# Kernel optimization log

Hardware: AMD Instinct MI355X
Metric: run time of the kernel (lower is better)

## Reference

```python
import jax, jax.numpy as jnp
import numpy as np

SQRT_2 = 1.414213
RT = 1.0  # Disk sets self.rt = 1.0
N_KPTS = 8192
M_KPTS = 8192
F_DIM = 256  # SuperPoint descriptor dim


def setup_inputs() -> dict:
    key = jax.random.key(0)
    k0, k1, k2, k3 = jax.random.split(key, 4)
    d0 = jax.random.normal(k0, (1, F_DIM, N_KPTS), dtype=jnp.float32)
    d1 = jax.random.normal(k1, (1, F_DIM, M_KPTS), dtype=jnp.float32)
    # distance_matrix assumes L2-normalized descriptors (normalize over F axis)
    d0 = d0 / jnp.linalg.norm(d0, axis=1, keepdims=True)
    d1 = d1 / jnp.linalg.norm(d1, axis=1, keepdims=True)
    kpts0 = jax.random.uniform(k2, (1, N_KPTS, 2), dtype=jnp.float32) * 480.0
    kpts1 = jax.random.uniform(k3, (1, M_KPTS, 2), dtype=jnp.float32) * 480.0
    return {"descriptors0": d0, "descriptors1": d1,
            "keypoints0": kpts0, "keypoints1": kpts1}


def _ratio_nn(dist):
    """Per-row nearest neighbor + Lowe ratio test. dist: [A, B].
    Returns (nn_idx [A] int32, pass_mask [A] bool)."""
    neg2, idx2 = jax.lax.top_k(-dist, 2)  # two smallest distances per row
    d1, d2 = -neg2[:, 0], -neg2[:, 1]
    return idx2[:, 0], (d1 / d2) < RT


def reference(descriptors0, descriptors1, keypoints0, keypoints1):
    fs0 = descriptors0[0].T  # [N, F]
    fs1 = descriptors1[0].T  # [M, F]
    # cosine -> L2-on-unit-sphere distance matrix, clamped as in the source
    dist = SQRT_2 * jnp.sqrt(jnp.clip(1.0 - fs0 @ fs1.T, 1e-6, None))  # [N, M]

    fwd_nn, fwd_ok = _ratio_nn(dist)    # [N]
    bck_nn, bck_ok = _ratio_nn(dist.T)  # [M]

    # mutual NN: (i, fwd_nn[i]) is kept iff the backward pass produced the
    # flipped pair (i, fwd_nn[i]) too -> same as counts==2 in the torch merge
    n = fs0.shape[0]
    mutual = fwd_ok & bck_ok[fwd_nn] & (bck_nn[fwd_nn] == jnp.arange(n))

    indices0 = jnp.where(mutual, fwd_nn, -1)[None, :].astype(jnp.int32)  # [1, N]
    mscores0 = jnp.where(indices0 > 0, 1, 0).astype(jnp.int32)           # [1, N]
    matches1 = jnp.full(keypoints1.shape[:-1], -1, dtype=jnp.int32)      # [1, M]
    mscores1 = jnp.zeros(keypoints1.shape[:-1], dtype=keypoints1.dtype)  # [1, M]
    return indices0, matches1, mscores0, mscores1
```

## Files before the change

kernel.cpp:

```cpp
#include <hip/hip_runtime.h>
#include <float.h>

#define NPTS 8192
#define MPTS 8192
#define FDIM 256

#define BM 128
#define BN 128
#define BK 64
#define TCT (MPTS / BN)
#define TRT (NPTS / BM)

typedef unsigned short ushort_t;
typedef unsigned int u32;
typedef __attribute__((ext_vector_type(8))) short short8;
typedef __attribute__((ext_vector_type(4))) float floatx4;

struct T2 { float s1, s2; int i1; };

__device__ __forceinline__ T2 t2_sent() { T2 a; a.s1 = -FLT_MAX; a.s2 = -FLT_MAX; a.i1 = 0; return a; }

__device__ __forceinline__ T2 t2_merge(T2 a, T2 b) {
    T2 r;
    r.s1 = fmaxf(a.s1, b.s1);
    r.i1 = (b.s1 > a.s1) ? b.i1 : a.i1;
    r.s2 = fmaxf(fminf(a.s1, b.s1), fmaxf(a.s2, b.s2));
    return r;
}
__device__ __forceinline__ T2 t2_make4(float v0, float v1, float v2, float v3,
                                       int i0, int i1_, int i2, int i3) {
    float lo01 = fminf(v0, v1), hi01 = fmaxf(v0, v1);
    float lo23 = fminf(v2, v3), hi23 = fmaxf(v2, v3);
    int a01 = (v1 > v0) ? i1_ : i0;
    int a23 = (v3 > v2) ? i3 : i2;
    T2 r;
    r.s1 = fmaxf(hi01, hi23);
    r.i1 = (hi23 > hi01) ? a23 : a01;
    r.s2 = fmaxf(fminf(hi01, hi23), fmaxf(lo01, lo23));
    return r;
}
__device__ __forceinline__ float4 t2_pack(T2 a) {
    return make_float4(a.s1, a.s2, __int_as_float(a.i1), 0.0f);
}
__device__ __forceinline__ T2 t2_unpack(float4 v) {
    T2 a; a.s1 = v.x; a.s2 = v.y; a.i1 = __float_as_int(v.z); return a;
}
__device__ __forceinline__ T2 t2_shfl_xor(T2 a, int m) {
    T2 r; r.s1 = __shfl_xor(a.s1, m); r.s2 = __shfl_xor(a.s2, m); r.i1 = __shfl_xor(a.i1, m);
    return r;
}

__device__ __forceinline__ float bf2f(ushort_t u) {
    union { u32 i; float f; } v; v.i = ((u32)u) << 16; return v.f;
}
__device__ __forceinline__ ushort_t f2bf_rtne(float x) {
    u32 u = __float_as_uint(x);
    u32 r = u + 0x7FFFu + ((u >> 16) & 1u);
    return (ushort_t)(r >> 16);
}

__global__ __launch_bounds__(256) void transpose_split(
    const float* __restrict__ s0, const float* __restrict__ s1,
    ushort_t* __restrict__ hi0, ushort_t* __restrict__ lo0,
    ushort_t* __restrict__ hi1, ushort_t* __restrict__ lo1)
{
    __shared__ ushort_t hiS[64][66];
    __shared__ ushort_t loS[64][66];
    const float* src = blockIdx.z ? s1 : s0;
    ushort_t* hiT = blockIdx.z ? hi1 : hi0;
    ushort_t* loT = blockIdx.z ? lo1 : lo0;
    const int t = threadIdx.x;
    const int n0 = blockIdx.x * 64, f0 = blockIdx.y * 64;

#pragma unroll
    for (int p = 0; p < 4; p++) {
        int fl = (t >> 4) + p * 16;
        int nl = (t & 15) * 4;
        float4 x = *(const float4*)&src[(size_t)(f0 + fl) * NPTS + n0 + nl];
        float xs[4] = {x.x, x.y, x.z, x.w};
#pragma unroll
        for (int e = 0; e < 4; e++) {
            ushort_t hb = f2bf_rtne(xs[e]);
            ushort_t lb = f2bf_rtne(xs[e] - bf2f(hb));
            hiS[nl + e][fl] = hb;
            loS[nl + e][fl] = lb;
        }
    }
    __syncthreads();
#pragma unroll
    for (int p = 0; p < 8; p++) {
        int nl = (t >> 5) + p * 8;
        int fp = (t & 31) * 2;
        u32 hw = (u32)hiS[nl][fp] | ((u32)hiS[nl][fp + 1] << 16);
        u32 lw = (u32)loS[nl][fp] | ((u32)loS[nl][fp + 1] << 16);
        size_t o = (size_t)(n0 + nl) * FDIM + f0 + fp;
        *(u32*)&hiT[o] = hw;
        *(u32*)&loT[o] = lw;
    }
}

#define GLDS(g, l) __builtin_amdgcn_global_load_lds( \
    (const __attribute__((address_space(1))) void*)(g), \
    (__attribute__((address_space(3))) void*)(l), 16, 0, 0)

__global__ __launch_bounds__(256, 2) void gemm_top2(
    const ushort_t* __restrict__ hiA, const ushort_t* __restrict__ loA,
    const ushort_t* __restrict__ hiB, const ushort_t* __restrict__ loB,
    float4* __restrict__ rowPart, float4* __restrict__ colPart)
{
    __shared__ char smem[65536];
    ushort_t* Ah = (ushort_t*)smem;
    ushort_t* Bh = (ushort_t*)(smem + 16384);
    ushort_t* Al = (ushort_t*)(smem + 32768);
    ushort_t* Bl = (ushort_t*)(smem + 49152);
    float* scrS1 = (float*)smem;
    float* scrS2 = (float*)(smem + 8448);
    int*   scrI  = (int*)(smem + 16896);
    float4* redC = (float4*)(smem + 25600);

    const int t = threadIdx.x;
    const int lane = t & 63, lc = lane & 15, q = lane >> 4;
    const int w = t >> 6, wx = w & 1, wy = w >> 1;
    const int ctile = blockIdx.x, rtile = blockIdx.y;
    const int n0 = rtile * BM, m0 = ctile * BN;

    floatx4 acc[4][4];
#pragma unroll
    for (int i = 0; i < 4; i++)
#pragma unroll
        for (int j = 0; j < 4; j++) acc[i][j] = (floatx4)0.0f;

    int srcOff[4];
#pragma unroll
    for (int cc = 0; cc < 4; cc++) {
        int L = cc * 256 + t;
        int row = L >> 3;
        int g = (L & 7) ^ (row & 7);
        srcOff[cc] = row * FDIM + g * 8;
    }
    const ushort_t* bAh = hiA + (size_t)n0 * FDIM;
    const ushort_t* bAl = loA + (size_t)n0 * FDIM;
    const ushort_t* bBh = hiB + (size_t)m0 * FDIM;
    const ushort_t* bBl = loB + (size_t)m0 * FDIM;

    int aoff[4][2], boff[4][2];
#pragma unroll
    for (int i = 0; i < 4; i++) {
        int ra = wy * 64 + i * 16 + lc;
        int rb = wx * 64 + i * 16 + lc;
#pragma unroll
        for (int s = 0; s < 2; s++) {
            aoff[i][s] = ra * BK + (((s * 4 + q) ^ (ra & 7)) * 8);
            boff[i][s] = rb * BK + (((s * 4 + q) ^ (rb & 7)) * 8);
        }
    }

    for (int k0 = 0; k0 < FDIM; k0 += BK) {
        if (k0) __syncthreads();
#pragma unroll
        for (int cc = 0; cc < 4; cc++) {
            int so = srcOff[cc] + k0;
            int ld = (cc * 256 + t) * 8;
            GLDS(bAh + so, Ah + ld);
            GLDS(bBh + so, Bh + ld);
            GLDS(bAl + so, Al + ld);
            GLDS(bBl + so, Bl + ld);
        }
        __syncthreads();

#pragma unroll
        for (int s = 0; s < 2; s++) {
            short8 ah[4], bh[4], al[4], bl[4];
#pragma unroll
            for (int i = 0; i < 4; i++) {
                ah[i] = *(const short8*)&Ah[aoff[i][s]];
                al[i] = *(const short8*)&Al[aoff[i][s]];
            }
#pragma unroll
            for (int j = 0; j < 4; j++) {
                bh[j] = *(const short8*)&Bh[boff[j][s]];
                bl[j] = *(const short8*)&Bl[boff[j][s]];
            }
#pragma unroll
            for (int i = 0; i < 4; i++)
#pragma unroll
                for (int j = 0; j < 4; j++) {
                    acc[i][j] = __builtin_amdgcn_mfma_f32_16x16x32_bf16(ah[i], bh[j], acc[i][j], 0, 0, 0);
                    acc[i][j] = __builtin_amdgcn_mfma_f32_16x16x32_bf16(ah[i], bl[j], acc[i][j], 0, 0, 0);
                    acc[i][j] = __builtin_amdgcn_mfma_f32_16x16x32_bf16(al[i], bh[j], acc[i][j], 0, 0, 0);
                }
        }
    }

    T2 colT[4];
#pragma unroll
    for (int j = 0; j < 4; j++) colT[j] = t2_sent();
    T2 rowT[4][4];

    const int cb = m0 + wx * 64 + lc;
#pragma unroll
    for (int i = 0; i < 4; i++) {
#pragma unroll
        for (int r = 0; r < 4; r++)
            rowT[i][r] = t2_make4(acc[i][0][r], acc[i][1][r], acc[i][2][r], acc[i][3][r],
                                  cb, cb + 16, cb + 32, cb + 48);
        const int rb = n0 + wy * 64 + i * 16 + q * 4;
#pragma unroll
        for (int j = 0; j < 4; j++)
            colT[j] = t2_merge(colT[j],
                t2_make4(acc[i][j][0], acc[i][j][1], acc[i][j][2], acc[i][j][3],
                         rb, rb + 1, rb + 2, rb + 3));
    }

#pragma unroll
    for (int j = 0; j < 4; j++) {
        colT[j] = t2_merge(colT[j], t2_shfl_xor(colT[j], 16));
        colT[j] = t2_merge(colT[j], t2_shfl_xor(colT[j], 32));
        if (q == 0) redC[(wx * 64 + j * 16 + lc) * 2 + wy] = t2_pack(colT[j]);
    }

#pragma unroll
    for (int round = 0; round < 2; round++) {
        __syncthreads();
        if (wy == round) {
#pragma unroll
            for (int i = 0; i < 4; i++)
#pragma unroll
                for (int r = 0; r < 4; r++) {
                    int row = i * 16 + q * 4 + r;
                    int col = (lc << 1) | wx;
                    int slot = row * 33 + ((col + row + 9 * q) & 31);
                    scrS1[slot] = rowT[i][r].s1;
                    scrS2[slot] = rowT[i][r].s2;
                    scrI[slot]  = rowT[i][r].i1;
                }
        }
        __syncthreads();
        {
            int row = t >> 2, chunk = t & 3;
            T2 a = t2_sent();
#pragma unroll
            for (int s = 0; s < 8; s++) {
                int slot = row * 33 + ((chunk << 3) | s);
                T2 b; b.s1 = scrS1[slot]; b.s2 = scrS2[slot]; b.i1 = scrI[slot];
                a = t2_merge(a, b);
            }
            a = t2_merge(a, t2_shfl_xor(a, 1));
            a = t2_merge(a, t2_shfl_xor(a, 2));
            if (chunk == 0)
                rowPart[(size_t)ctile * NPTS + n0 + round * 64 + row] = t2_pack(a);
        }
    }

    __syncthreads();
    if (t < 128) {
        T2 m = t2_unpack(redC[t * 2 + 0]);
        m = t2_merge(m, t2_unpack(redC[t * 2 + 1]));
        colPart[(size_t)rtile * MPTS + m0 + t] = t2_pack(m);
    }
}

__global__ __launch_bounds__(256) void reduce_final(
    const float4* __restrict__ rowPart, const float4* __restrict__ colPart,
    float* __restrict__ out)
{
    __shared__ float4 sh[4][64];
    __shared__ int shFwd[64];
    __shared__ int shOk[64];
    const int t = threadIdx.x, nl = t & 63, sub = t >> 6;
    const int n = blockIdx.x * 64 + nl;

    T2 a = t2_sent();
#pragma unroll
    for (int k = 0; k < 16; k++)
        a = t2_merge(a, t2_unpack(rowPart[(size_t)(sub * 16 + k) * NPTS + n]));
    sh[sub][nl] = t2_pack(a);
    __syncthreads();
    if (t < 64) {
        T2 r = t2_unpack(sh[0][t]);
        r = t2_merge(r, t2_unpack(sh[1][t]));
        r = t2_merge(r, t2_unpack(sh[2][t]));
        r = t2_merge(r, t2_unpack(sh[3][t]));
        float c1 = fmaxf(1.0f - r.s1, 1e-6f), c2 = fmaxf(1.0f - r.s2, 1e-6f);
        float d1 = 1.414213f * sqrtf(c1), d2 = 1.414213f * sqrtf(c2);
        shFwd[t] = r.i1;
        shOk[t]  = ((d1 / d2) < 1.0f) ? 1 : 0;
    }
    __syncthreads();
    const int fw = shFwd[nl];
    T2 c = t2_sent();
#pragma unroll
    for (int k = 0; k < 16; k++)
        c = t2_merge(c, t2_unpack(colPart[(size_t)(sub * 16 + k) * MPTS + fw]));
    sh[sub][nl] = t2_pack(c);
    __syncthreads();
    if (t < 64) {
        T2 r = t2_unpack(sh[0][t]);
        r = t2_merge(r, t2_unpack(sh[1][t]));
        r = t2_merge(r, t2_unpack(sh[2][t]));
        r = t2_merge(r, t2_unpack(sh[3][t]));
        float c1 = fmaxf(1.0f - r.s1, 1e-6f), c2 = fmaxf(1.0f - r.s2, 1e-6f);
        float d1 = 1.414213f * sqrtf(c1), d2 = 1.414213f * sqrtf(c2);
        bool bok = (d1 / d2) < 1.0f;
        int nn = blockIdx.x * 64 + t;
        bool mutual = (shOk[t] != 0) && bok && (r.i1 == nn);
        int idx0 = mutual ? shFwd[t] : -1;
        out[nn]             = (float)idx0;
        out[NPTS + nn]      = -1.0f;
        out[2 * NPTS + nn]  = (idx0 > 0) ? 1.0f : 0.0f;
        out[3 * NPTS + nn]  = 0.0f;
    }
}

extern "C" void kernel_launch(void* const* d_in, const int* in_sizes, int n_in,
                              void* d_out, int out_size, void* d_ws, size_t ws_size,
                              hipStream_t stream)
{
    const float* d0 = (const float*)d_in[0];
    const float* d1 = (const float*)d_in[1];

    char* ws = (char*)d_ws;
    const size_t matB = (size_t)NPTS * FDIM * sizeof(ushort_t);
    ushort_t* hiA = (ushort_t*)(ws);
    ushort_t* loA = (ushort_t*)(ws + matB);
    ushort_t* hiB = (ushort_t*)(ws + 2 * matB);
    ushort_t* loB = (ushort_t*)(ws + 3 * matB);
    char* p = ws + 4 * matB;
    const size_t rowBytes = (size_t)TCT * NPTS * sizeof(float4);
    float4* rowPart = (float4*)p;
    float4* colPart = (float4*)(p + rowBytes);

    dim3 gt(NPTS / 64, FDIM / 64, 2);
    transpose_split<<<gt, 256, 0, stream>>>(d0, d1, hiA, loA, hiB, loB);

    dim3 g1(TCT, TRT);
    gemm_top2<<<g1, 256, 0, stream>>>(hiA, loA, hiB, loB, rowPart, colPart);
    reduce_final<<<NPTS / 64, 256, 0, stream>>>(rowPart, colPart, (float*)d_out);
}
```

Baseline: 179.8 us.

## Use 256x256 tiles with double-buffered LDS pipeline and 8-wave blocks

Enlarges the GEMM tile to 256x256 with 512 threads and BK=32. Global-to-LDS loads for the next K step are double-buffered and issued during MFMA phases, using explicit waitcnt, barriers and priority hints. Larger tiles cut redundant operand reloads and halve the partial top-2 outputs that reduce_final must merge. In exchange, LDS use grows to 128 KB and each thread carries 128 accumulator registers, which limits occupancy.

New measurement: 243.8 us. 35.6% more time.

```diff
diff --git a/kernel.cpp b/kernel.cpp
--- a/kernel.cpp
+++ b/kernel.cpp
@@ -5,9 +5,10 @@
 #define MPTS 8192
 #define FDIM 256
 
-#define BM 128
-#define BN 128
-#define BK 64
+#define BM 256
+#define BN 256
+#define BK 32
+#define KSTEPS (FDIM / BK)
 #define TCT (MPTS / BN)
 #define TRT (NPTS / BM)
 
@@ -103,136 +104,178 @@
     (const __attribute__((address_space(1))) void*)(g), \
     (__attribute__((address_space(3))) void*)(l), 16, 0, 0)
 
-__global__ __launch_bounds__(256, 2) void gemm_top2(
+#define STAGE(k0v, bufp, cc) do { \
+    int _so = srcOff[cc] + (k0v); \
+    char* _lb = (bufp) + ldsOff[cc]; \
+    GLDS(bAh + _so, _lb); \
+    GLDS(bBh + _so, _lb + 16384); \
+    GLDS(bAl + _so, _lb + 32768); \
+    GLDS(bBl + _so, _lb + 49152); \
+} while (0)
+
+#define READ_PH1(Pb) do { \
+    _Pragma("unroll") for (int i = 0; i < 4; i++) { \
+        ah[i] = *(const short8*)((Pb) + aBase + i * 1024); \
+        al[i] = *(const short8*)((Pb) + 32768 + aBase + i * 1024); \
+    } \
+    _Pragma("unroll") for (int j = 0; j < 4; j++) { \
+        bh[j] = *(const short8*)((Pb) + 16384 + bBase + j * 1024); \
+        bl[j] = *(const short8*)((Pb) + 49152 + bBase + j * 1024); \
+    } \
+} while (0)
+
+#define MFMA16(AH, AL, IOFF) do { \
+    _Pragma("unroll") for (int i = 0; i < 4; i++) \
+    _Pragma("unroll") for (int j = 0; j < 4; j++) { \
+        acc[(IOFF) + i][j] = __builtin_amdgcn_mfma_f32_16x16x32_bf16(AH[i], bh[j], acc[(IOFF) + i][j], 0, 0, 0); \
+        acc[(IOFF) + i][j] = __builtin_amdgcn_mfma_f32_16x16x32_bf16(AH[i], bl[j], acc[(IOFF) + i][j], 0, 0, 0); \
+        acc[(IOFF) + i][j] = __builtin_amdgcn_mfma_f32_16x16x32_bf16(AL[i], bh[j], acc[(IOFF) + i][j], 0, 0, 0); \
+    } \
+} while (0)
+
+#define KSTEP(ksv, Pb, Qb) do { \
+    const int kn_ = ((ksv) + 1) * BK; \
+    STAGE(kn_, Qb, 0); \
+    asm volatile("s_waitcnt vmcnt(4)" ::: "memory"); \
+    __builtin_amdgcn_s_barrier(); \
+    READ_PH1(Pb); \
+    asm volatile("s_waitcnt lgkmcnt(0)" ::: "memory"); \
+    __builtin_amdgcn_sched_barrier(0); \
+    __builtin_amdgcn_s_setprio(1); \
+    MFMA16(ah, al, 0); \
+    __builtin_amdgcn_s_setprio(0); \
+    __builtin_amdgcn_s_barrier(); \
+    _Pragma("unroll") for (int i = 0; i < 4; i++) { \
+        ch[i] = *(const short8*)((Pb) + aBase + (i + 4) * 1024); \
+        cl[i] = *(const short8*)((Pb) + 32768 + aBase + (i + 4) * 1024); \
+    } \
+    STAGE(kn_, Qb, 1); \
+    __builtin_amdgcn_s_barrier(); \
+    asm volatile("s_waitcnt lgkmcnt(0)" ::: "memory"); \
+    __builtin_amdgcn_sched_barrier(0); \
+    __builtin_amdgcn_s_setprio(1); \
+    MFMA16(ch, cl, 4); \
+    __builtin_amdgcn_s_setprio(0); \
+    __builtin_amdgcn_s_barrier(); \
+} while (0)
+
+__global__ __launch_bounds__(512, 2) void gemm_top2(
     const ushort_t* __restrict__ hiA, const ushort_t* __restrict__ loA,
     const ushort_t* __restrict__ hiB, const ushort_t* __restrict__ loB,
     float4* __restrict__ rowPart, float4* __restrict__ colPart)
 {
-    __shared__ char smem[65536];
-    ushort_t* Ah = (ushort_t*)smem;
-    ushort_t* Bh = (ushort_t*)(smem + 16384);
-    ushort_t* Al = (ushort_t*)(smem + 32768);
-    ushort_t* Bl = (ushort_t*)(smem + 49152);
-    float* scrS1 = (float*)smem;
-    float* scrS2 = (float*)(smem + 8448);
-    int*   scrI  = (int*)(smem + 16896);
-    float4* redC = (float4*)(smem + 25600);
-
+    __shared__ char smem[131072];
     const int t = threadIdx.x;
     const int lane = t & 63, lc = lane & 15, q = lane >> 4;
-    const int w = t >> 6, wx = w & 1, wy = w >> 1;
+    const int w = t >> 6, wx = w & 3, wy = w >> 2;
     const int ctile = blockIdx.x, rtile = blockIdx.y;
     const int n0 = rtile * BM, m0 = ctile * BN;
 
-    floatx4 acc[4][4];
-#pragma unroll
-    for (int i = 0; i < 4; i++)
+    floatx4 acc[8][4];
+#pragma unroll
+    for (int i = 0; i < 8; i++)
 #pragma unroll
         for (int j = 0; j < 4; j++) acc[i][j] = (floatx4)0.0f;
 
-    int srcOff[4];
-#pragma unroll
-    for (int cc = 0; cc < 4; cc++) {
-        int L = cc * 256 + t;
-        int row = L >> 3;
-        int g = (L & 7) ^ (row & 7);
+    int srcOff[2], ldsOff[2];
+#pragma unroll
+    for (int cc = 0; cc < 2; cc++) {
+        int L = cc * 512 + t;
+        int row = L >> 2;
+        int g = (L & 3) ^ (row & 3);
         srcOff[cc] = row * FDIM + g * 8;
+        ldsOff[cc] = L * 16;
     }
     const ushort_t* bAh = hiA + (size_t)n0 * FDIM;
     const ushort_t* bAl = loA + (size_t)n0 * FDIM;
     const ushort_t* bBh = hiB + (size_t)m0 * FDIM;
     const ushort_t* bBl = loB + (size_t)m0 * FDIM;
 
-    int aoff[4][2], boff[4][2];
-#pragma unroll
-    for (int i = 0; i < 4; i++) {
-        int ra = wy * 64 + i * 16 + lc;
-        int rb = wx * 64 + i * 16 + lc;
-#pragma unroll
-        for (int s = 0; s < 2; s++) {
-            aoff[i][s] = ra * BK + (((s * 4 + q) ^ (ra & 7)) * 8);
-            boff[i][s] = rb * BK + (((s * 4 + q) ^ (rb & 7)) * 8);
-        }
-    }
-
-    for (int k0 = 0; k0 < FDIM; k0 += BK) {
-        if (k0) __syncthreads();
-#pragma unroll
-        for (int cc = 0; cc < 4; cc++) {
-            int so = srcOff[cc] + k0;
-            int ld = (cc * 256 + t) * 8;
-            GLDS(bAh + so, Ah + ld);
-            GLDS(bBh + so, Bh + ld);
-            GLDS(bAl + so, Al + ld);
-            GLDS(bBl + so, Bl + ld);
-        }
-        __syncthreads();
-
-#pragma unroll
-        for (int s = 0; s < 2; s++) {
-            short8 ah[4], bh[4], al[4], bl[4];
-#pragma unroll
-            for (int i = 0; i < 4; i++) {
-                ah[i] = *(const short8*)&Ah[aoff[i][s]];
-                al[i] = *(const short8*)&Al[aoff[i][s]];
-            }
-#pragma unroll
-            for (int j = 0; j < 4; j++) {
-                bh[j] = *(const short8*)&Bh[boff[j][s]];
-                bl[j] = *(const short8*)&Bl[boff[j][s]];
-            }
-#pragma unroll
-            for (int i = 0; i < 4; i++)
-#pragma unroll
-                for (int j = 0; j < 4; j++) {
-                    acc[i][j] = __builtin_amdgcn_mfma_f32_16x16x32_bf16(ah[i], bh[j], acc[i][j], 0, 0, 0);
-                    acc[i][j] = __builtin_amdgcn_mfma_f32_16x16x32_bf16(ah[i], bl[j], acc[i][j], 0, 0, 0);
-                    acc[i][j] = __builtin_amdgcn_mfma_f32_16x16x32_bf16(al[i], bh[j], acc[i][j], 0, 0, 0);
-                }
-        }
-    }
-
-    T2 colT[4];
-#pragma unroll
-    for (int j = 0; j < 4; j++) colT[j] = t2_sent();
-    T2 rowT[4][4];
-
+    const int xa = (q ^ (lc & 3)) * 16;
+    const int aBase = (wy * 128 + lc) * 64 + xa;
+    const int bBase = (wx * 64 + lc) * 64 + xa;
+
+    short8 ah[4], al[4], bh[4], bl[4], ch[4], cl[4];
+
+    char* buf0 = smem;
+    char* buf1 = smem + 65536;
+    STAGE(0, buf0, 0);
+    STAGE(0, buf0, 1);
+#pragma unroll 1
+    for (int kp = 0; kp < 3; kp++) {
+        KSTEP(2 * kp, buf0, buf1);
+        KSTEP(2 * kp + 1, buf1, buf0);
+    }
+    KSTEP(6, buf0, buf1);
+    {
+        char* Pb = buf1;
+        asm volatile("s_waitcnt vmcnt(0)" ::: "memory");
+        __builtin_amdgcn_s_barrier();
+        READ_PH1(Pb);
+        asm volatile("s_waitcnt lgkmcnt(0)" ::: "memory");
+        __builtin_amdgcn_sched_barrier(0);
+        __builtin_amdgcn_s_setprio(1);
+        MFMA16(ah, al, 0);
+        __builtin_amdgcn_s_setprio(0);
+#pragma unroll
+        for (int i = 0; i < 4; i++) {
+            ch[i] = *(const short8*)(Pb + aBase + (i + 4) * 1024);
+            cl[i] = *(const short8*)(Pb + 32768 + aBase + (i + 4) * 1024);
+        }
+        asm volatile("s_waitcnt lgkmcnt(0)" ::: "memory");
+        __builtin_amdgcn_sched_barrier(0);
+        __builtin_amdgcn_s_setprio(1);
+        MFMA16(ch, cl, 4);
+        __builtin_amdgcn_s_setprio(0);
+    }
+    __syncthreads();
+
+    float4* redC = (float4*)smem;
+    {
+        T2 colT[4];
+#pragma unroll
+        for (int j = 0; j < 4; j++) colT[j] = t2_sent();
+#pragma unroll
+        for (int i = 0; i < 8; i++) {
+            const int rb = n0 + wy * 128 + i * 16 + q * 4;
+#pragma unroll
+            for (int j = 0; j < 4; j++)
+                colT[j] = t2_merge(colT[j],
+                    t2_make4(acc[i][j][0], acc[i][j][1], acc[i][j][2], acc[i][j][3],
+                             rb, rb + 1, rb + 2, rb + 3));
+        }
+#pragma unroll
+        for (int j = 0; j < 4; j++) {
+            colT[j] = t2_merge(colT[j], t2_shfl_xor(colT[j], 16));
+            colT[j] = t2_merge(colT[j], t2_shfl_xor(colT[j], 32));
+            if (q == 0) redC[(wx * 64 + j * 16 + lc) * 2 + wy] = t2_pack(colT[j]);
+        }
+    }
+    __syncthreads();
+    if (t < 256) {
+        T2 m = t2_unpack(redC[t * 2 + 0]);
+        m = t2_merge(m, t2_unpack(redC[t * 2 + 1]));
+        colPart[(size_t)rtile * MPTS + m0 + t] = t2_pack(m);
+    }
+
+    float* scrS1 = (float*)smem;
+    float* scrS2 = (float*)(smem + 33280);
+    int*   scrI  = (int*)(smem + 66560);
     const int cb = m0 + wx * 64 + lc;
-#pragma unroll
-    for (int i = 0; i < 4; i++) {
-#pragma unroll
-        for (int r = 0; r < 4; r++)
-            rowT[i][r] = t2_make4(acc[i][0][r], acc[i][1][r], acc[i][2][r], acc[i][3][r],
-                                  cb, cb + 16, cb + 32, cb + 48);
-        const int rb = n0 + wy * 64 + i * 16 + q * 4;
-#pragma unroll
-        for (int j = 0; j < 4; j++)
-            colT[j] = t2_merge(colT[j],
-                t2_make4(acc[i][j][0], acc[i][j][1], acc[i][j][2], acc[i][j][3],
-                         rb, rb + 1, rb + 2, rb + 3));
-    }
-
-#pragma unroll
-    for (int j = 0; j < 4; j++) {
-        colT[j] = t2_merge(colT[j], t2_shfl_xor(colT[j], 16));
-        colT[j] = t2_merge(colT[j], t2_shfl_xor(colT[j], 32));
-        if (q == 0) redC[(wx * 64 + j * 16 + lc) * 2 + wy] = t2_pack(colT[j]);
-    }
-
+    const int pp = wx * 16 + lc;
 #pragma unroll
     for (int round = 0; round < 2; round++) {
         __syncthreads();
         if (wy == round) {
 #pragma unroll
-            for (int i = 0; i < 4; i++)
+            for (int i = 0; i < 8; i++)
 #pragma unroll
                 for (int r = 0; r < 4; r++) {
                     int row = i * 16 + q * 4 + r;
-                    int col = (lc << 1) | wx;
-                    int slot = row * 33 + ((col + row + 9 * q) & 31);
-                    scrS1[slot] = rowT[i][r].s1;
-                    scrS2[slot] = rowT[i][r].s2;
-                    scrI[slot]  = rowT[i][r].i1;
+                    T2 v = t2_make4(acc[i][0][r], acc[i][1][r], acc[i][2][r], acc[i][3][r],
+                                    cb, cb + 16, cb + 32, cb + 48);
+                    int slot = row * 65 + ((pp + row) & 63);
+                    scrS1[slot] = v.s1; scrS2[slot] = v.s2; scrI[slot] = v.i1;
                 }
         }
         __syncthreads();
@@ -240,23 +283,16 @@
             int row = t >> 2, chunk = t & 3;
             T2 a = t2_sent();
 #pragma unroll
-            for (int s = 0; s < 8; s++) {
-                int slot = row * 33 + ((chunk << 3) | s);
+            for (int s = 0; s < 16; s++) {
+                int slot = row * 65 + ((((chunk << 4) | s) + row) & 63);
                 T2 b; b.s1 = scrS1[slot]; b.s2 = scrS2[slot]; b.i1 = scrI[slot];
                 a = t2_merge(a, b);
             }
             a = t2_merge(a, t2_shfl_xor(a, 1));
             a = t2_merge(a, t2_shfl_xor(a, 2));
             if (chunk == 0)
-                rowPart[(size_t)ctile * NPTS + n0 + round * 64 + row] = t2_pack(a);
-        }
-    }
-
-    __syncthreads();
-    if (t < 128) {
-        T2 m = t2_unpack(redC[t * 2 + 0]);
-        m = t2_merge(m, t2_unpack(redC[t * 2 + 1]));
-        colPart[(size_t)rtile * MPTS + m0 + t] = t2_pack(m);
+                rowPart[(size_t)ctile * NPTS + n0 + round * 128 + row] = t2_pack(a);
+        }
     }
 }
 
@@ -272,8 +308,8 @@
 
     T2 a = t2_sent();
 #pragma unroll
-    for (int k = 0; k < 16; k++)
-        a = t2_merge(a, t2_unpack(rowPart[(size_t)(sub * 16 + k) * NPTS + n]));
+    for (int k = 0; k < 8; k++)
+        a = t2_merge(a, t2_unpack(rowPart[(size_t)(sub * 8 + k) * NPTS + n]));
     sh[sub][nl] = t2_pack(a);
     __syncthreads();
     if (t < 64) {
@@ -290,8 +326,8 @@
     const int fw = shFwd[nl];
     T2 c = t2_sent();
 #pragma unroll
-    for (int k = 0; k < 16; k++)
-        c = t2_merge(c, t2_unpack(colPart[(size_t)(sub * 16 + k) * MPTS + fw]));
+    for (int k = 0; k < 8; k++)
+        c = t2_merge(c, t2_unpack(colPart[(size_t)(sub * 8 + k) * MPTS + fw]));
     sh[sub][nl] = t2_pack(c);
     __syncthreads();
     if (t < 64) {
@@ -334,6 +370,6 @@
     transpose_split<<<gt, 256, 0, stream>>>(d0, d1, hiA, loA, hiB, loB);
 
     dim3 g1(TCT, TRT);
-    gemm_top2<<<g1, 256, 0, stream>>>(hiA, loA, hiB, loB, rowPart, colPart);
+    gemm_top2<<<g1, 512, 0, stream>>>(hiA, loA, hiB, loB, rowPart, colPart);
     reduce_final<<<NPTS / 64, 256, 0, stream>>>(rowPart, colPart, (float*)d_out);
 }
```

## Double-buffer LDS with BK=32 to overlap global loads and MFMA

Applied to the files above, without the earlier changes.

Halves the K tile to 32 and splits the 64 KB LDS into two 32 KB buffers, so the global-to-LDS loads for the next K step are issued before the MFMAs of the current step run. Manual vmcnt/lgkmcnt waits, raw barriers and sched_barriers replace __syncthreads to control ordering, and the LDS swizzle is redone for the 64-byte rows. This aims to hide global load latency behind the hi/lo split-bf16 MFMA work, at the cost of more barriers per K step and fragile hand-written wait counts.

New measurement: 191.9 us. 6.8% more time.

```diff
diff --git a/kernel.cpp b/kernel.cpp
--- a/kernel.cpp
+++ b/kernel.cpp
@@ -7,7 +7,7 @@
 
 #define BM 128
 #define BN 128
-#define BK 64
+#define BK 32
 #define TCT (MPTS / BN)
 #define TRT (NPTS / BM)
 
@@ -103,16 +103,53 @@
     (const __attribute__((address_space(1))) void*)(g), \
     (__attribute__((address_space(3))) void*)(l), 16, 0, 0)
 
+#define STAGE(k0v, bufp) do { \
+    _Pragma("unroll") for (int cc = 0; cc < 2; cc++) { \
+        int _so = srcOff[cc] + (k0v); \
+        char* _lb = (bufp) + ldsOff[cc]; \
+        GLDS(bAh + _so, _lb); \
+        GLDS(bBh + _so, _lb + 8192); \
+        GLDS(bAl + _so, _lb + 16384); \
+        GLDS(bBl + _so, _lb + 24576); \
+    } \
+} while (0)
+
+#define READ_ALL(Pb) do { \
+    _Pragma("unroll") for (int i = 0; i < 4; i++) { \
+        ah[i] = *(const short8*)((Pb) + aoff[i]); \
+        al[i] = *(const short8*)((Pb) + 16384 + aoff[i]); \
+        bh[i] = *(const short8*)((Pb) + 8192 + boff[i]); \
+        bl[i] = *(const short8*)((Pb) + 24576 + boff[i]); \
+    } \
+} while (0)
+
+#define MFMA48 do { \
+    _Pragma("unroll") for (int i = 0; i < 4; i++) \
+    _Pragma("unroll") for (int j = 0; j < 4; j++) { \
+        acc[i][j] = __builtin_amdgcn_mfma_f32_16x16x32_bf16(ah[i], bh[j], acc[i][j], 0, 0, 0); \
+        acc[i][j] = __builtin_amdgcn_mfma_f32_16x16x32_bf16(ah[i], bl[j], acc[i][j], 0, 0, 0); \
+        acc[i][j] = __builtin_amdgcn_mfma_f32_16x16x32_bf16(al[i], bh[j], acc[i][j], 0, 0, 0); \
+    } \
+} while (0)
+
+#define KSTEP(ksv, Pb, Qb) do { \
+    STAGE(((ksv) + 1) * BK, Qb); \
+    asm volatile("s_waitcnt vmcnt(8)" ::: "memory"); \
+    __builtin_amdgcn_s_barrier(); \
+    READ_ALL(Pb); \
+    asm volatile("s_waitcnt lgkmcnt(0)" ::: "memory"); \
+    __builtin_amdgcn_sched_barrier(0); \
+    MFMA48; \
+    __builtin_amdgcn_sched_barrier(0); \
+    __builtin_amdgcn_s_barrier(); \
+} while (0)
+
 __global__ __launch_bounds__(256, 2) void gemm_top2(
     const ushort_t* __restrict__ hiA, const ushort_t* __restrict__ loA,
     const ushort_t* __restrict__ hiB, const ushort_t* __restrict__ loB,
     float4* __restrict__ rowPart, float4* __restrict__ colPart)
 {
     __shared__ char smem[65536];
-    ushort_t* Ah = (ushort_t*)smem;
-    ushort_t* Bh = (ushort_t*)(smem + 16384);
-    ushort_t* Al = (ushort_t*)(smem + 32768);
-    ushort_t* Bl = (ushort_t*)(smem + 49152);
     float* scrS1 = (float*)smem;
     float* scrS2 = (float*)(smem + 8448);
     int*   scrI  = (int*)(smem + 16896);
@@ -130,67 +167,48 @@
 #pragma unroll
         for (int j = 0; j < 4; j++) acc[i][j] = (floatx4)0.0f;
 
-    int srcOff[4];
-#pragma unroll
-    for (int cc = 0; cc < 4; cc++) {
+    int srcOff[2], ldsOff[2];
+#pragma unroll
+    for (int cc = 0; cc < 2; cc++) {
         int L = cc * 256 + t;
-        int row = L >> 3;
-        int g = (L & 7) ^ (row & 7);
+        int row = L >> 2;
+        int g = (L & 3) ^ ((L >> 3) & 3);
         srcOff[cc] = row * FDIM + g * 8;
+        ldsOff[cc] = L * 16;
     }
     const ushort_t* bAh = hiA + (size_t)n0 * FDIM;
     const ushort_t* bAl = loA + (size_t)n0 * FDIM;
     const ushort_t* bBh = hiB + (size_t)m0 * FDIM;
     const ushort_t* bBl = loB + (size_t)m0 * FDIM;
 
-    int aoff[4][2], boff[4][2];
+    const int xa = (q ^ ((lc >> 1) & 3)) * 16;
+    int aoff[4], boff[4];
 #pragma unroll
     for (int i = 0; i < 4; i++) {
-        int ra = wy * 64 + i * 16 + lc;
-        int rb = wx * 64 + i * 16 + lc;
-#pragma unroll
-        for (int s = 0; s < 2; s++) {
-            aoff[i][s] = ra * BK + (((s * 4 + q) ^ (ra & 7)) * 8);
-            boff[i][s] = rb * BK + (((s * 4 + q) ^ (rb & 7)) * 8);
-        }
-    }
-
-    for (int k0 = 0; k0 < FDIM; k0 += BK) {
-        if (k0) __syncthreads();
-#pragma unroll
-        for (int cc = 0; cc < 4; cc++) {
-            int so = srcOff[cc] + k0;
-            int ld = (cc * 256 + t) * 8;
-            GLDS(bAh + so, Ah + ld);
-            GLDS(bBh + so, Bh + ld);
-            GLDS(bAl + so, Al + ld);
-            GLDS(bBl + so, Bl + ld);
-        }
-        __syncthreads();
-
-#pragma unroll
-        for (int s = 0; s < 2; s++) {
-            short8 ah[4], bh[4], al[4], bl[4];
-#pragma unroll
-            for (int i = 0; i < 4; i++) {
-                ah[i] = *(const short8*)&Ah[aoff[i][s]];
-                al[i] = *(const short8*)&Al[aoff[i][s]];
-            }
-#pragma unroll
-            for (int j = 0; j < 4; j++) {
-                bh[j] = *(const short8*)&Bh[boff[j][s]];
-                bl[j] = *(const short8*)&Bl[boff[j][s]];
-            }
-#pragma unroll
-            for (int i = 0; i < 4; i++)
-#pragma unroll
-                for (int j = 0; j < 4; j++) {
-                    acc[i][j] = __builtin_amdgcn_mfma_f32_16x16x32_bf16(ah[i], bh[j], acc[i][j], 0, 0, 0);
-                    acc[i][j] = __builtin_amdgcn_mfma_f32_16x16x32_bf16(ah[i], bl[j], acc[i][j], 0, 0, 0);
-                    acc[i][j] = __builtin_amdgcn_mfma_f32_16x16x32_bf16(al[i], bh[j], acc[i][j], 0, 0, 0);
-                }
-        }
-    }
+        aoff[i] = (wy * 64 + i * 16 + lc) * 64 + xa;
+        boff[i] = (wx * 64 + i * 16 + lc) * 64 + xa;
+    }
+
+    short8 ah[4], al[4], bh[4], bl[4];
+
+    char* buf0 = smem;
+    char* buf1 = smem + 32768;
+    STAGE(0, buf0);
+#pragma unroll 1
+    for (int kp = 0; kp < 3; kp++) {
+        KSTEP(2 * kp, buf0, buf1);
+        KSTEP(2 * kp + 1, buf1, buf0);
+    }
+    KSTEP(6, buf0, buf1);
+    {
+        asm volatile("s_waitcnt vmcnt(0)" ::: "memory");
+        __builtin_amdgcn_s_barrier();
+        READ_ALL(buf1);
+        asm volatile("s_waitcnt lgkmcnt(0)" ::: "memory");
+        __builtin_amdgcn_sched_barrier(0);
+        MFMA48;
+    }
+    __syncthreads();
 
     T2 colT[4];
 #pragma unroll
```
